# Performance work log

Measured on AMD Instinct MI355X. Metric: run time of the kernel, lower is better.

The kernel has to match this reference:

```python
import jax, jax.numpy as jnp
import numpy as np

N_NODES = 100000
N_EDGES = 625000
D = 128
DEPTH = 2
BN_EPS = 1e-5


def setup_inputs() -> dict:
    key = jax.random.key(0)
    ks = jax.random.split(key, 8)
    x = jax.random.normal(ks[0], (N_NODES, D), dtype=jnp.float32)
    edge_index = jax.random.randint(ks[1], (2, N_EDGES), 0, N_NODES, dtype=jnp.int64)
    edge_weight = jax.random.uniform(ks[2], (N_EDGES,), dtype=jnp.float32)
    s = 1.0 / np.sqrt(D)
    W_lin = jax.random.uniform(ks[3], (DEPTH, D, D), jnp.float32, -s, s)
    W_gcn = jax.random.uniform(ks[4], (DEPTH, D, D), jnp.float32, -s, s)
    gamma = jnp.ones((DEPTH, D), jnp.float32)
    beta = jnp.zeros((DEPTH, D), jnp.float32)
    return {"x": x, "edge_index": edge_index, "edge_weight": edge_weight,
            "W_lin": W_lin, "W_gcn": W_gcn, "gamma": gamma, "beta": beta}


def reference(x, edge_index, edge_weight, W_lin, W_gcn, gamma, beta):
    n = x.shape[0]
    row, col = edge_index[0], edge_index[1]  # source, target
    # gcn_norm with add_self_loops=False: deg over targets, symmetric normalization
    deg = jax.ops.segment_sum(edge_weight, col, num_segments=n)
    dinv = jnp.where(deg > 0, jax.lax.rsqrt(deg), 0.0)
    norm = dinv[row] * edge_weight * dinv[col]  # [E]

    for i in range(DEPTH):
        hl = x @ W_lin[i].T                       # parallel linear branch
        hg = x @ W_gcn[i].T                       # GCNConv linear
        msg = norm[:, None] * hg[row]             # [E, D] messages
        hr = jax.ops.segment_sum(msg, col, num_segments=n)
        h = hl + hr
        # BatchNorm1d, training mode (batch statistics, biased variance)
        mu = jnp.mean(h, axis=0)
        var = jnp.mean((h - mu) ** 2, axis=0)
        h = (h - mu) * jax.lax.rsqrt(var + BN_EPS) * gamma[i] + beta[i]
        x = jnp.maximum(h, 0.0) if i != DEPTH - 1 else h
    return x
```

## Files before the change

### kernel.cpp

```cpp
#include <hip/hip_runtime.h>

#define NN 100000
#define NE 625000
#define DD 128
#define CAP 32
#define NREP 8

#define CONVB 12500
#define WPACKB 256
#define FILL2B ((NE / 2 + 255) / 256)
#define GB ((NN + 63) / 64)

typedef __attribute__((ext_vector_type(8))) short bf16x8;
typedef __attribute__((ext_vector_type(4))) float f32x4;

static __device__ __forceinline__ unsigned short f2bf(float f) {
    union { float f; unsigned u; } v; v.f = f;
    unsigned u = v.u + 0x7fffu + ((v.u >> 16) & 1u);
    return (unsigned short)(u >> 16);
}
static __device__ __forceinline__ float bflo(unsigned u) { return __uint_as_float(u << 16); }
static __device__ __forceinline__ float bfhi(unsigned u) { return __uint_as_float(u & 0xffff0000u); }

static __device__ __forceinline__ void foldLDS(const float* __restrict__ stats,
                                               const float* __restrict__ gamma,
                                               const float* __restrict__ beta,
                                               float* sSc, float* sSh, int t) {
    if (t < 128) {
        float sum = 0.f, sq = 0.f;
        #pragma unroll
        for (int rp = 0; rp < NREP; rp++) {
            sum += stats[rp * 256 + t];
            sq  += stats[rp * 256 + 128 + t];
        }
        float mu = sum * (1.0f / NN);
        float var = sq * (1.0f / NN) - mu * mu;
        float is = rsqrtf(var + 1e-5f);
        float sc = is * gamma[t];
        sSc[t] = sc;
        sSh[t] = beta[t] - mu * sc;
    }
}

__global__ __launch_bounds__(256) void k_pre(const float* __restrict__ x,
                                             unsigned* __restrict__ Xb2,
                                             const float* __restrict__ Wl,
                                             const float* __restrict__ Wg,
                                             unsigned short* __restrict__ wp,
                                             const int* __restrict__ row,
                                             const int* __restrict__ col,
                                             const float* __restrict__ w,
                                             int* __restrict__ cnt,
                                             int2* __restrict__ ebuf) {
    int b = blockIdx.x, t = threadIdx.x;
    if (b < FILL2B) {
        int id = b * 256 + t;
        if (id < NE / 2) {
            int e = id * 2;
            int2 rr = *(const int2*)&row[e];
            int2 cc = *(const int2*)&col[e];
            float2 ww = *(const float2*)&w[e];
            int p0 = atomicAdd(&cnt[cc.x], 1);
            int p1 = atomicAdd(&cnt[cc.y], 1);
            if (p0 < CAP) {
                int2 v; v.x = rr.x; v.y = __float_as_int(ww.x);
                ebuf[(size_t)cc.x * CAP + p0] = v;
            }
            if (p1 < CAP) {
                int2 v; v.x = rr.y; v.y = __float_as_int(ww.y);
                ebuf[(size_t)cc.y * CAP + p1] = v;
            }
        }
    } else if (b < FILL2B + WPACKB) {
        int idx = (b - FILL2B) * 256 + t;
        int l = idx >> 15;
        int rem = idx & 32767;
        int n = rem >> 8;
        int k = rem & 255;
        float v = (k < 128) ? Wl[(size_t)l * DD * DD + n * DD + k]
                            : Wg[(size_t)l * DD * DD + n * DD + (k - 128)];
        int wv = n >> 5;
        int tt = (n >> 4) & 1;
        int i  = n & 15;
        int ss = k >> 5;
        int q  = (k >> 3) & 3;
        int j  = k & 7;
        size_t off = ((size_t)((((l * 4 + wv) * 2 + tt) * 8 + ss)) * 64 + q * 16 + i) * 8 + j;
        wp[off] = f2bf(v);
    } else {
        size_t i = (size_t)(b - FILL2B - WPACKB) * 256 + t;
        size_t base = i * 4;
        float4 v = *(const float4*)&x[base];
        uint2 o;
        o.x = (unsigned)f2bf(v.x) | ((unsigned)f2bf(v.y) << 16);
        o.y = (unsigned)f2bf(v.z) | ((unsigned)f2bf(v.w) << 16);
        *(uint2*)&Xb2[i * 2] = o;
    }
}

__global__ __launch_bounds__(256) void k_dinvb(const int* __restrict__ cnt,
                                               const int2* __restrict__ ebuf,
                                               float* __restrict__ dinv) {
    int t = threadIdx.x;
    int node = blockIdx.x * 32 + (t >> 3);
    int l = t & 7;
    int c = cnt[node]; if (c > CAP) c = CAP;
    float s = 0.f;
    for (int p = l; p < c; p += 8) s += __int_as_float(ebuf[(size_t)node * CAP + p].y);
    s += __shfl_down(s, 4, 8);
    s += __shfl_down(s, 2, 8);
    s += __shfl_down(s, 1, 8);
    if (l == 0) dinv[node] = (s > 0.f) ? rsqrtf(s) : 0.f;
}

template<int LAYER>
__global__ __launch_bounds__(256) void k_gatherP(const int* __restrict__ cnt,
                                                 const int2* __restrict__ ebuf,
                                                 const float* __restrict__ dinv,
                                                 const unsigned* __restrict__ X2,
                                                 const float* __restrict__ stats,
                                                 const float* __restrict__ gamma,
                                                 const float* __restrict__ beta,
                                                 unsigned* __restrict__ P2) {
    __shared__ float sSc[128], sSh[128];
    const int t = threadIdx.x;
    const int wave = t >> 6;
    const int lane = t & 63;
    float scx = 0.f, scy = 0.f, shx = 0.f, shy = 0.f;
    if (LAYER) {
        foldLDS(stats, gamma, beta, sSc, sSh, t);
        __syncthreads();
        scx = sSc[2 * lane]; scy = sSc[2 * lane + 1];
        shx = sSh[2 * lane]; shy = sSh[2 * lane + 1];
    }

    const int node0 = blockIdx.x * 8 + wave * 2;
    const int node1 = node0 + 1;
    int c0 = cnt[node0]; if (c0 > CAP) c0 = CAP;
    int c1 = cnt[node1]; if (c1 > CAP) c1 = CAP;
    const int2* eb0 = ebuf + (size_t)node0 * CAP;
    const int2* eb1 = ebuf + (size_t)node1 * CAP;
    float ax0 = 0.f, ay0 = 0.f, ax1 = 0.f, ay1 = 0.f;

    auto chunk4 = [&](const int2* __restrict__ eb, int p, float& ax, float& ay) {
        int2 e0 = eb[p], e1 = eb[p + 1], e2 = eb[p + 2], e3 = eb[p + 3];
        float w0 = __int_as_float(e0.y) * dinv[e0.x];
        float w1 = __int_as_float(e1.y) * dinv[e1.x];
        float w2 = __int_as_float(e2.y) * dinv[e2.x];
        float w3 = __int_as_float(e3.y) * dinv[e3.x];
        unsigned u0 = X2[(size_t)e0.x * 64 + lane];
        unsigned u1 = X2[(size_t)e1.x * 64 + lane];
        unsigned u2 = X2[(size_t)e2.x * 64 + lane];
        unsigned u3 = X2[(size_t)e3.x * 64 + lane];
        float x0 = bflo(u0), y0 = bfhi(u0);
        float x1 = bflo(u1), y1 = bfhi(u1);
        float x2 = bflo(u2), y2 = bfhi(u2);
        float x3 = bflo(u3), y3 = bfhi(u3);
        if (LAYER) {
            x0 = fmaxf(x0 * scx + shx, 0.f); y0 = fmaxf(y0 * scy + shy, 0.f);
            x1 = fmaxf(x1 * scx + shx, 0.f); y1 = fmaxf(y1 * scy + shy, 0.f);
            x2 = fmaxf(x2 * scx + shx, 0.f); y2 = fmaxf(y2 * scy + shy, 0.f);
            x3 = fmaxf(x3 * scx + shx, 0.f); y3 = fmaxf(y3 * scy + shy, 0.f);
        }
        ax += w0 * x0 + w1 * x1 + w2 * x2 + w3 * x3;
        ay += w0 * y0 + w1 * y1 + w2 * y2 + w3 * y3;
    };
    auto edge1 = [&](const int2* __restrict__ eb, int p, float& ax, float& ay) {
        int2 e0 = eb[p];
        float w0 = __int_as_float(e0.y) * dinv[e0.x];
        unsigned u0 = X2[(size_t)e0.x * 64 + lane];
        float x0 = bflo(u0), y0 = bfhi(u0);
        if (LAYER) {
            x0 = fmaxf(x0 * scx + shx, 0.f); y0 = fmaxf(y0 * scy + shy, 0.f);
        }
        ax += w0 * x0;
        ay += w0 * y0;
    };

    const int mc = (c0 < c1) ? c0 : c1;
    int p = 0;
    for (; p + 3 < mc; p += 4) {
        chunk4(eb0, p, ax0, ay0);
        chunk4(eb1, p, ax1, ay1);
    }
    int p0 = p, p1 = p;
    for (; p0 + 3 < c0; p0 += 4) chunk4(eb0, p0, ax0, ay0);
    for (; p0 < c0; p0++)        edge1(eb0, p0, ax0, ay0);
    for (; p1 + 3 < c1; p1 += 4) chunk4(eb1, p1, ax1, ay1);
    for (; p1 < c1; p1++)        edge1(eb1, p1, ax1, ay1);

    float dn0 = dinv[node0], dn1 = dinv[node1];
    ax0 *= dn0; ay0 *= dn0;
    ax1 *= dn1; ay1 *= dn1;
    P2[(size_t)node0 * 64 + lane] = (unsigned)f2bf(ax0) | ((unsigned)f2bf(ay0) << 16);
    P2[(size_t)node1 * 64 + lane] = (unsigned)f2bf(ax1) | ((unsigned)f2bf(ay1) << 16);
}

template<int LAYER>
__global__ __launch_bounds__(256) void k_gemm_s(const unsigned short* Xin,
                                                const unsigned short* P,
                                                const unsigned short* __restrict__ wp,
                                                const float* __restrict__ statsIn,
                                                const float* __restrict__ gammaIn,
                                                const float* __restrict__ betaIn,
                                                unsigned short* Hout,
                                                float* __restrict__ statsOut) {
    __shared__ __align__(16) char smem[34816];
    unsigned short* sAv = (unsigned short*)smem;
    unsigned short* sBv = (unsigned short*)smem;
    float* red = (float*)(smem + 17408);
    float* sSc = (float*)(smem + 33792);
    float* sSh = (float*)(smem + 34304);

    const int t = threadIdx.x;
    const int wave = t >> 6;
    const int lane = t & 63;
    const int i16 = lane & 15;
    const int quad = lane >> 4;
    const int rowBase = blockIdx.x * 64;

    if (LAYER == 1) {
        foldLDS(statsIn, gammaIn, betaIn, sSc, sSh, t);
        __syncthreads();
    }

    bf16x8 wf[2][8];
    #pragma unroll
    for (int tt = 0; tt < 2; tt++)
        #pragma unroll
        for (int ss = 0; ss < 8; ss++) {
            size_t off = ((size_t)(((wave * 2 + tt) * 8 + ss)) * 64 + quad * 16 + i16) * 8;
            wf[tt][ss] = *(const bf16x8*)&wp[off];
        }

    #pragma unroll
    for (int rep = 0; rep < 4; rep++) {
        int lin = rep * 2048 + t * 8;
        int r = lin >> 7, c = lin & 127;
        int rr = rowBase + r; if (rr >= NN) rr = NN - 1;
        uint4 u = *(const uint4*)&Xin[(size_t)rr * DD + c];
        if (LAYER == 1) {
            float4 sc0 = *(const float4*)&sSc[c];
            float4 sc1 = *(const float4*)&sSc[c + 4];
            float4 sh0 = *(const float4*)&sSh[c];
            float4 sh1 = *(const float4*)&sSh[c + 4];
            float v0 = fmaxf(bflo(u.x) * sc0.x + sh0.x, 0.f);
            float v1 = fmaxf(bfhi(u.x) * sc0.y + sh0.y, 0.f);
            float v2 = fmaxf(bflo(u.y) * sc0.z + sh0.z, 0.f);
            float v3 = fmaxf(bfhi(u.y) * sc0.w + sh0.w, 0.f);
            float v4 = fmaxf(bflo(u.z) * sc1.x + sh1.x, 0.f);
            float v5 = fmaxf(bfhi(u.z) * sc1.y + sh1.y, 0.f);
            float v6 = fmaxf(bflo(u.w) * sc1.z + sh1.z, 0.f);
            float v7 = fmaxf(bfhi(u.w) * sc1.w + sh1.w, 0.f);
            u.x = (unsigned)f2bf(v0) | ((unsigned)f2bf(v1) << 16);
            u.y = (unsigned)f2bf(v2) | ((unsigned)f2bf(v3) << 16);
            u.z = (unsigned)f2bf(v4) | ((unsigned)f2bf(v5) << 16);
            u.w = (unsigned)f2bf(v6) | ((unsigned)f2bf(v7) << 16);
        }
        *(uint4*)&sAv[r * 264 + c] = u;
    }
    #pragma unroll
    for (int rep = 0; rep < 4; rep++) {
        int lin = rep * 2048 + t * 8;
        int r = lin >> 7, c = lin & 127;
        int rr = rowBase + r; if (rr >= NN) rr = NN - 1;
        uint4 u = *(const uint4*)&P[(size_t)rr * DD + c];
        *(uint4*)&sAv[r * 264 + 128 + c] = u;
    }
    __syncthreads();

    f32x4 acc[4][2] = {{{0.f,0.f,0.f,0.f}}};
    #pragma unroll
    for (int ss = 0; ss < 8; ss++) {
        bf16x8 af[4];
        #pragma unroll
        for (int mt = 0; mt < 4; mt++)
            af[mt] = *(const bf16x8*)&sAv[(mt * 16 + i16) * 264 + ss * 32 + quad * 8];
        #pragma unroll
        for (int mt = 0; mt < 4; mt++)
            #pragma unroll
            for (int tt = 0; tt < 2; tt++)
                acc[mt][tt] = __builtin_amdgcn_mfma_f32_16x16x32_bf16(
                    af[mt], wf[tt][ss], acc[mt][tt], 0, 0, 0);
    }

    __syncthreads();
    #pragma unroll
    for (int mt = 0; mt < 4; mt++)
        #pragma unroll
        for (int r = 0; r < 4; r++) {
            int row = mt * 16 + quad * 4 + r;
            #pragma unroll
            for (int tt = 0; tt < 2; tt++)
                sBv[row * 136 + wave * 32 + tt * 16 + i16] = f2bf(acc[mt][tt][r]);
        }
    __syncthreads();

    float s[8] = {0.f,0.f,0.f,0.f,0.f,0.f,0.f,0.f};
    float q[8] = {0.f,0.f,0.f,0.f,0.f,0.f,0.f,0.f};
    const int cg = t & 15;
    #pragma unroll
    for (int it = 0; it < 4; it++) {
        int row = it * 16 + (t >> 4);
        int gr = rowBase + row;
        uint4 v = *(const uint4*)&sBv[row * 136 + cg * 8];
        float m = (gr < NN) ? 1.f : 0.f;
        if (gr < NN) *(uint4*)&Hout[(size_t)gr * DD + cg * 8] = v;
        float e0 = bflo(v.x) * m, e1 = bfhi(v.x) * m;
        float e2 = bflo(v.y) * m, e3 = bfhi(v.y) * m;
        float e4 = bflo(v.z) * m, e5 = bfhi(v.z) * m;
        float e6 = bflo(v.w) * m, e7 = bfhi(v.w) * m;
        s[0] += e0; q[0] += e0 * e0;  s[1] += e1; q[1] += e1 * e1;
        s[2] += e2; q[2] += e2 * e2;  s[3] += e3; q[3] += e3 * e3;
        s[4] += e4; q[4] += e4 * e4;  s[5] += e5; q[5] += e5 * e5;
        s[6] += e6; q[6] += e6 * e6;  s[7] += e7; q[7] += e7 * e7;
    }
    {
        int ro = t >> 4;
        #pragma unroll
        for (int j = 0; j < 8; j++) {
            red[(ro * 16 + cg) * 16 + j]     = s[j];
            red[(ro * 16 + cg) * 16 + 8 + j] = q[j];
        }
    }
    __syncthreads();
    {
        int colx = t & 127;
        int type = t >> 7;
        float tot = 0.f;
        #pragma unroll
        for (int ro = 0; ro < 16; ro++)
            tot += red[(ro * 16 + (colx >> 3)) * 16 + type * 8 + (colx & 7)];
        atomicAdd(&statsOut[(blockIdx.x & (NREP - 1)) * 256 + type * 128 + colx], tot);
    }
}

__global__ __launch_bounds__(256) void k_apply_out(const unsigned* __restrict__ H2,
                                                   const float* __restrict__ stats,
                                                   const float* __restrict__ gamma,
                                                   const float* __restrict__ beta,
                                                   float* __restrict__ out) {
    __shared__ __align__(16) float sSc[128];
    __shared__ __align__(16) float sSh[128];
    int t = threadIdx.x;
    foldLDS(stats, gamma, beta, sSc, sSh, t);
    __syncthreads();
    size_t i = (size_t)blockIdx.x * 256 + t;
    size_t base = i * 4;
    int c = (int)(base & 127);
    uint2 u = *(const uint2*)&H2[i * 2];
    float4 sc = *(const float4*)&sSc[c];
    float4 sh = *(const float4*)&sSh[c];
    float4 o;
    o.x = bflo(u.x) * sc.x + sh.x;
    o.y = bfhi(u.x) * sc.y + sh.y;
    o.z = bflo(u.y) * sc.z + sh.z;
    o.w = bfhi(u.y) * sc.w + sh.w;
    *(float4*)&out[base] = o;
}

extern "C" void kernel_launch(void* const* d_in, const int* in_sizes, int n_in,
                              void* d_out, int out_size, void* d_ws, size_t ws_size,
                              hipStream_t stream) {
    const float* x_in  = (const float*)d_in[0];
    const int*   ei    = (const int*)d_in[1];
    const float* ew    = (const float*)d_in[2];
    const float* Wl    = (const float*)d_in[3];
    const float* Wg    = (const float*)d_in[4];
    const float* gamma = (const float*)d_in[5];
    const float* beta  = (const float*)d_in[6];
    float* out = (float*)d_out;

    char* p = (char*)d_ws;
    unsigned short* bufA = (unsigned short*)p; p += (size_t)NN * DD * 2;
    unsigned short* bufB = (unsigned short*)p; p += (size_t)NN * DD * 2;
    int2* ebuf  = (int2*)p;  p += (size_t)NN * CAP * 8;
    int*   cnt    = (int*)p;   p += (size_t)NN * 4;
    float* stats0 = (float*)p; p += NREP * 256 * 4;
    float* stats1 = (float*)p; p += NREP * 256 * 4;
    float* dinv   = (float*)p; p += 400000;
    unsigned short* wpack = (unsigned short*)p; p += 65536 * 2;

    const int* row = ei;
    const int* col = ei + NE;

    hipMemsetAsync(cnt, 0, (size_t)NN * 4 + 2 * NREP * 256 * 4, stream);
    k_pre<<<FILL2B + WPACKB + CONVB, 256, 0, stream>>>(
        x_in, (unsigned*)bufA, Wl, Wg, wpack, row, col, ew, cnt, ebuf);
    k_dinvb<<<NN / 32, 256, 0, stream>>>(cnt, ebuf, dinv);

    k_gatherP<0><<<NN / 8, 256, 0, stream>>>(cnt, ebuf, dinv, (const unsigned*)bufA,
                                             nullptr, nullptr, nullptr, (unsigned*)bufB);
    k_gemm_s<0><<<GB, 256, 0, stream>>>(bufA, bufB, wpack,
                                        nullptr, nullptr, nullptr, bufA, stats0);

    k_gatherP<1><<<NN / 8, 256, 0, stream>>>(cnt, ebuf, dinv, (const unsigned*)bufA,
                                             stats0, gamma, beta, (unsigned*)bufB);
    k_gemm_s<1><<<GB, 256, 0, stream>>>(bufA, bufB, wpack + 32768,
                                        stats0, gamma, beta, bufB, stats1);

    k_apply_out<<<NN * DD / 1024, 256, 0, stream>>>((const unsigned*)bufB, stats1,
                                                    gamma + DD, beta + DD, out);
}
```

Baseline: 292.2 us.

## Split GEMM K-loop into two LDS phases to shrink smem and raise occupancy

The fused GEMM now processes the X half and the aggregated-P half of K in two sequential phases that reuse a 64x136 LDS tile, not one 64x264 tile. Weight fragments are loaded per half, which lowers register use, and launch bounds request 5 blocks per CU. The BN statistics reduction now uses wave shuffles before a smaller LDS reduction. The preprocessing kernel is split into separate edge-fill and conversion kernels. The cost is extra barriers and a serialized load-compute sequence inside each block.

```diff
diff --git a/kernel.cpp b/kernel.cpp
--- a/kernel.cpp
+++ b/kernel.cpp
@@ -42,37 +42,38 @@
     }
 }
 
-__global__ __launch_bounds__(256) void k_pre(const float* __restrict__ x,
-                                             unsigned* __restrict__ Xb2,
-                                             const float* __restrict__ Wl,
-                                             const float* __restrict__ Wg,
-                                             unsigned short* __restrict__ wp,
-                                             const int* __restrict__ row,
-                                             const int* __restrict__ col,
-                                             const float* __restrict__ w,
-                                             int* __restrict__ cnt,
-                                             int2* __restrict__ ebuf) {
+__global__ __launch_bounds__(256) void k_fill(const int* __restrict__ row,
+                                              const int* __restrict__ col,
+                                              const float* __restrict__ w,
+                                              int* __restrict__ cnt,
+                                              int2* __restrict__ ebuf) {
+    int id = blockIdx.x * 256 + threadIdx.x;
+    if (id < NE / 2) {
+        int e = id * 2;
+        int2 rr = *(const int2*)&row[e];
+        int2 cc = *(const int2*)&col[e];
+        float2 ww = *(const float2*)&w[e];
+        int p0 = atomicAdd(&cnt[cc.x], 1);
+        int p1 = atomicAdd(&cnt[cc.y], 1);
+        if (p0 < CAP) {
+            int2 v; v.x = rr.x; v.y = __float_as_int(ww.x);
+            ebuf[(size_t)cc.x * CAP + p0] = v;
+        }
+        if (p1 < CAP) {
+            int2 v; v.x = rr.y; v.y = __float_as_int(ww.y);
+            ebuf[(size_t)cc.y * CAP + p1] = v;
+        }
+    }
+}
+
+__global__ __launch_bounds__(256) void k_conv(const float* __restrict__ x,
+                                              unsigned* __restrict__ Xb2,
+                                              const float* __restrict__ Wl,
+                                              const float* __restrict__ Wg,
+                                              unsigned short* __restrict__ wp) {
     int b = blockIdx.x, t = threadIdx.x;
-    if (b < FILL2B) {
-        int id = b * 256 + t;
-        if (id < NE / 2) {
-            int e = id * 2;
-            int2 rr = *(const int2*)&row[e];
-            int2 cc = *(const int2*)&col[e];
-            float2 ww = *(const float2*)&w[e];
-            int p0 = atomicAdd(&cnt[cc.x], 1);
-            int p1 = atomicAdd(&cnt[cc.y], 1);
-            if (p0 < CAP) {
-                int2 v; v.x = rr.x; v.y = __float_as_int(ww.x);
-                ebuf[(size_t)cc.x * CAP + p0] = v;
-            }
-            if (p1 < CAP) {
-                int2 v; v.x = rr.y; v.y = __float_as_int(ww.y);
-                ebuf[(size_t)cc.y * CAP + p1] = v;
-            }
-        }
-    } else if (b < FILL2B + WPACKB) {
-        int idx = (b - FILL2B) * 256 + t;
+    if (b < WPACKB) {
+        int idx = b * 256 + t;
         int l = idx >> 15;
         int rem = idx & 32767;
         int n = rem >> 8;
@@ -88,7 +89,7 @@
         size_t off = ((size_t)((((l * 4 + wv) * 2 + tt) * 8 + ss)) * 64 + q * 16 + i) * 8 + j;
         wp[off] = f2bf(v);
     } else {
-        size_t i = (size_t)(b - FILL2B - WPACKB) * 256 + t;
+        size_t i = (size_t)(b - WPACKB) * 256 + t;
         size_t base = i * 4;
         float4 v = *(const float4*)&x[base];
         uint2 o;
@@ -197,20 +198,19 @@
 }
 
 template<int LAYER>
-__global__ __launch_bounds__(256) void k_gemm_s(const unsigned short* Xin,
-                                                const unsigned short* P,
-                                                const unsigned short* __restrict__ wp,
-                                                const float* __restrict__ statsIn,
-                                                const float* __restrict__ gammaIn,
-                                                const float* __restrict__ betaIn,
-                                                unsigned short* Hout,
-                                                float* __restrict__ statsOut) {
-    __shared__ __align__(16) char smem[34816];
-    unsigned short* sAv = (unsigned short*)smem;
-    unsigned short* sBv = (unsigned short*)smem;
-    float* red = (float*)(smem + 17408);
-    float* sSc = (float*)(smem + 33792);
-    float* sSh = (float*)(smem + 34304);
+__global__ __launch_bounds__(256, 5) void k_gemm_s(const unsigned short* Xin,
+                                                   const unsigned short* P,
+                                                   const unsigned short* __restrict__ wp,
+                                                   const float* __restrict__ statsIn,
+                                                   const float* __restrict__ gammaIn,
+                                                   const float* __restrict__ betaIn,
+                                                   unsigned short* Hout,
+                                                   float* __restrict__ statsOut) {
+    __shared__ __align__(16) char smem[22528];
+    unsigned short* sA = (unsigned short*)smem;
+    float* red2 = (float*)(smem + 17408);
+    float* sSc = (float*)(smem + 21504);
+    float* sSh = (float*)(smem + 22016);
 
     const int t = threadIdx.x;
     const int wave = t >> 6;
@@ -224,14 +224,7 @@
         __syncthreads();
     }
 
-    bf16x8 wf[2][8];
-    #pragma unroll
-    for (int tt = 0; tt < 2; tt++)
-        #pragma unroll
-        for (int ss = 0; ss < 8; ss++) {
-            size_t off = ((size_t)(((wave * 2 + tt) * 8 + ss)) * 64 + quad * 16 + i16) * 8;
-            wf[tt][ss] = *(const bf16x8*)&wp[off];
-        }
+    f32x4 acc[4][2] = {{{0.f,0.f,0.f,0.f}}};
 
     #pragma unroll
     for (int rep = 0; rep < 4; rep++) {
@@ -257,34 +250,68 @@
             u.z = (unsigned)f2bf(v4) | ((unsigned)f2bf(v5) << 16);
             u.w = (unsigned)f2bf(v6) | ((unsigned)f2bf(v7) << 16);
         }
-        *(uint4*)&sAv[r * 264 + c] = u;
-    }
+        *(uint4*)&sA[r * 136 + c] = u;
+    }
+    __syncthreads();
+    {
+        bf16x8 wf[2][4];
+        #pragma unroll
+        for (int tt = 0; tt < 2; tt++)
+            #pragma unroll
+            for (int ss = 0; ss < 4; ss++) {
+                size_t off = ((size_t)(((wave * 2 + tt) * 8 + ss)) * 64 + quad * 16 + i16) * 8;
+                wf[tt][ss] = *(const bf16x8*)&wp[off];
+            }
+        #pragma unroll
+        for (int ss = 0; ss < 4; ss++) {
+            bf16x8 af[4];
+            #pragma unroll
+            for (int mt = 0; mt < 4; mt++)
+                af[mt] = *(const bf16x8*)&sA[(mt * 16 + i16) * 136 + ss * 32 + quad * 8];
+            #pragma unroll
+            for (int mt = 0; mt < 4; mt++)
+                #pragma unroll
+                for (int tt = 0; tt < 2; tt++)
+                    acc[mt][tt] = __builtin_amdgcn_mfma_f32_16x16x32_bf16(
+                        af[mt], wf[tt][ss], acc[mt][tt], 0, 0, 0);
+        }
+    }
+    __syncthreads();
+
     #pragma unroll
     for (int rep = 0; rep < 4; rep++) {
         int lin = rep * 2048 + t * 8;
         int r = lin >> 7, c = lin & 127;
         int rr = rowBase + r; if (rr >= NN) rr = NN - 1;
         uint4 u = *(const uint4*)&P[(size_t)rr * DD + c];
-        *(uint4*)&sAv[r * 264 + 128 + c] = u;
-    }
-    __syncthreads();
-
-    f32x4 acc[4][2] = {{{0.f,0.f,0.f,0.f}}};
-    #pragma unroll
-    for (int ss = 0; ss < 8; ss++) {
-        bf16x8 af[4];
-        #pragma unroll
-        for (int mt = 0; mt < 4; mt++)
-            af[mt] = *(const bf16x8*)&sAv[(mt * 16 + i16) * 264 + ss * 32 + quad * 8];
-        #pragma unroll
-        for (int mt = 0; mt < 4; mt++)
-            #pragma unroll
-            for (int tt = 0; tt < 2; tt++)
-                acc[mt][tt] = __builtin_amdgcn_mfma_f32_16x16x32_bf16(
-                    af[mt], wf[tt][ss], acc[mt][tt], 0, 0, 0);
-    }
-
-    __syncthreads();
+        *(uint4*)&sA[r * 136 + c] = u;
+    }
+    __syncthreads();
+    {
+        bf16x8 wf[2][4];
+        #pragma unroll
+        for (int tt = 0; tt < 2; tt++)
+            #pragma unroll
+            for (int ss = 0; ss < 4; ss++) {
+                size_t off = ((size_t)(((wave * 2 + tt) * 8 + ss + 4)) * 64 + quad * 16 + i16) * 8;
+                wf[tt][ss] = *(const bf16x8*)&wp[off];
+            }
+        #pragma unroll
+        for (int ss = 0; ss < 4; ss++) {
+            bf16x8 af[4];
+            #pragma unroll
+            for (int mt = 0; mt < 4; mt++)
+                af[mt] = *(const bf16x8*)&sA[(mt * 16 + i16) * 136 + ss * 32 + quad * 8];
+            #pragma unroll
+            for (int mt = 0; mt < 4; mt++)
+                #pragma unroll
+                for (int tt = 0; tt < 2; tt++)
+                    acc[mt][tt] = __builtin_amdgcn_mfma_f32_16x16x32_bf16(
+                        af[mt], wf[tt][ss], acc[mt][tt], 0, 0, 0);
+        }
+    }
+    __syncthreads();
+
     #pragma unroll
     for (int mt = 0; mt < 4; mt++)
         #pragma unroll
@@ -292,7 +319,7 @@
             int row = mt * 16 + quad * 4 + r;
             #pragma unroll
             for (int tt = 0; tt < 2; tt++)
-                sBv[row * 136 + wave * 32 + tt * 16 + i16] = f2bf(acc[mt][tt][r]);
+                sA[row * 136 + wave * 32 + tt * 16 + i16] = f2bf(acc[mt][tt][r]);
         }
     __syncthreads();
 
@@ -303,7 +330,7 @@
     for (int it = 0; it < 4; it++) {
         int row = it * 16 + (t >> 4);
         int gr = rowBase + row;
-        uint4 v = *(const uint4*)&sBv[row * 136 + cg * 8];
+        uint4 v = *(const uint4*)&sA[row * 136 + cg * 8];
         float m = (gr < NN) ? 1.f : 0.f;
         if (gr < NN) *(uint4*)&Hout[(size_t)gr * DD + cg * 8] = v;
         float e0 = bflo(v.x) * m, e1 = bfhi(v.x) * m;
@@ -315,22 +342,28 @@
         s[4] += e4; q[4] += e4 * e4;  s[5] += e5; q[5] += e5 * e5;
         s[6] += e6; q[6] += e6 * e6;  s[7] += e7; q[7] += e7 * e7;
     }
-    {
-        int ro = t >> 4;
+    #pragma unroll
+    for (int j = 0; j < 8; j++) {
+        s[j] += __shfl_xor(s[j], 16);
+        s[j] += __shfl_xor(s[j], 32);
+        q[j] += __shfl_xor(q[j], 16);
+        q[j] += __shfl_xor(q[j], 32);
+    }
+    if (lane < 16) {
         #pragma unroll
         for (int j = 0; j < 8; j++) {
-            red[(ro * 16 + cg) * 16 + j]     = s[j];
-            red[(ro * 16 + cg) * 16 + 8 + j] = q[j];
+            red2[(wave * 16 + lane) * 16 + j]     = s[j];
+            red2[(wave * 16 + lane) * 16 + 8 + j] = q[j];
         }
     }
     __syncthreads();
     {
         int colx = t & 127;
         int type = t >> 7;
-        float tot = 0.f;
-        #pragma unroll
-        for (int ro = 0; ro < 16; ro++)
-            tot += red[(ro * 16 + (colx >> 3)) * 16 + type * 8 + (colx & 7)];
+        int j = type * 8 + (colx & 7);
+        int cgx = colx >> 3;
+        float tot = red2[(0 * 16 + cgx) * 16 + j] + red2[(1 * 16 + cgx) * 16 + j]
+                  + red2[(2 * 16 + cgx) * 16 + j] + red2[(3 * 16 + cgx) * 16 + j];
         atomicAdd(&statsOut[(blockIdx.x & (NREP - 1)) * 256 + type * 128 + colx], tot);
     }
 }
@@ -385,8 +418,8 @@
     const int* col = ei + NE;
 
     hipMemsetAsync(cnt, 0, (size_t)NN * 4 + 2 * NREP * 256 * 4, stream);
-    k_pre<<<FILL2B + WPACKB + CONVB, 256, 0, stream>>>(
-        x_in, (unsigned*)bufA, Wl, Wg, wpack, row, col, ew, cnt, ebuf);
+    k_fill<<<FILL2B, 256, 0, stream>>>(row, col, ew, cnt, ebuf);
+    k_conv<<<WPACKB + CONVB, 256, 0, stream>>>(x_in, (unsigned*)bufA, Wl, Wg, wpack);
     k_dinvb<<<NN / 32, 256, 0, stream>>>(cnt, ebuf, dinv);
 
     k_gatherP<0><<<NN / 8, 256, 0, stream>>>(cnt, ebuf, dinv, (const unsigned*)bufA,
```

Measured after the change: 291.8 us. Within noise of the previous version (-0.1%).
